# Performance work log

Measured on AMD Instinct MI355X. Metric: run time of the kernel, lower is better.

## Reference

```python
import jax, jax.numpy as jnp
import numpy as np

DIM = 768
HEADS = 12
HEAD_DIM = DIM // HEADS
EPS = 1e-5

def setup_inputs() -> dict:
    key = jax.random.key(0)
    ks = jax.random.split(key, 12)
    s = 1.0 / np.sqrt(DIM)
    x = jax.random.normal(ks[0], (4, 2048, DIM), dtype=jnp.float32)
    Wq = jax.random.uniform(ks[1], (DIM, DIM), jnp.float32, -s, s)
    bq = jnp.zeros((DIM,), jnp.float32)
    Wk = jax.random.uniform(ks[2], (DIM, DIM), jnp.float32, -s, s)
    bk = jnp.zeros((DIM,), jnp.float32)
    Wv = jax.random.uniform(ks[3], (DIM, DIM), jnp.float32, -s, s)
    bv = jnp.zeros((DIM,), jnp.float32)
    W1 = jax.random.uniform(ks[4], (DIM, 2 * DIM), jnp.float32, -s, s)
    b1 = jnp.zeros((2 * DIM,), jnp.float32)
    s2 = 1.0 / np.sqrt(2 * DIM)
    W2 = jax.random.uniform(ks[5], (2 * DIM, DIM), jnp.float32, -s2, s2)
    b2 = jnp.zeros((DIM,), jnp.float32)
    gamma = jnp.ones((DIM,), jnp.float32)
    beta = jnp.zeros((DIM,), jnp.float32)
    return {"x": x, "Wq": Wq, "bq": bq, "Wk": Wk, "bk": bk, "Wv": Wv, "bv": bv,
            "W1": W1, "b1": b1, "W2": W2, "b2": b2, "gamma": gamma, "beta": beta}

def reference(x, Wq, bq, Wk, bk, Wv, bv, W1, b1, W2, b2, gamma, beta):
    B, S, _ = x.shape
    # QKV projections -> (B, H, S, Dh)
    q = (x @ Wq + bq).reshape(B, S, HEADS, HEAD_DIM).transpose(0, 2, 1, 3)
    k = (x @ Wk + bk).reshape(B, S, HEADS, HEAD_DIM).transpose(0, 2, 1, 3)
    v = (x @ Wv + bv).reshape(B, S, HEADS, HEAD_DIM).transpose(0, 2, 1, 3)
    scores = jnp.einsum('bhqd,bhkd->bhqk', q, k) / jnp.sqrt(jnp.float32(HEAD_DIM))
    attn = jax.nn.softmax(scores, axis=-1)  # dropout is identity in eval
    ctx = jnp.einsum('bhqk,bhkd->bhqd', attn, v)
    ctx = ctx.transpose(0, 2, 1, 3).reshape(B, S, DIM)
    # MLP
    out = jax.nn.relu(ctx @ W1 + b1) @ W2 + b2
    # residual + LayerNorm
    h = x + out
    mu = jnp.mean(h, axis=-1, keepdims=True)
    var = jnp.mean(jnp.square(h - mu), axis=-1, keepdims=True)
    return (h - mu) * jax.lax.rsqrt(var + EPS) * gamma + beta
```

## Files before the change

### kernel.cpp

```cpp
#include <hip/hip_runtime.h>
#include <stdint.h>

#define DIM 768
#define HDIM 64
#define NHEADS 12
#define SEQ 2048
#define BATCH 4
#define NTOK (BATCH*SEQ)
#define FF 1536
#define QSCALE 0.1803368801111204f

typedef __bf16 bf16x8 __attribute__((ext_vector_type(8)));
typedef float f32x4 __attribute__((ext_vector_type(4)));
typedef unsigned short u16;
typedef unsigned int u32;

static __device__ __forceinline__ u16 f2bf(float f) {
  u32 u = __float_as_uint(f);
  u32 r = (u + 0x7fffu + ((u >> 16) & 1u)) >> 16;
  return (u16)r;
}

static __device__ __forceinline__ void async16(const void* g, void* l) {
  __builtin_amdgcn_global_load_lds(
      (const __attribute__((address_space(1))) u32*)g,
      (__attribute__((address_space(3))) u32*)l, 16, 0, 0);
}


__global__ void conv_bf16(const float* __restrict__ in, u16* __restrict__ out, int n) {
  int i = (blockIdx.x * 256 + threadIdx.x) * 4;
  if (i < n) {
    float4 f = *(const float4*)(in + i);
    uint2 o;
    o.x = (u32)f2bf(f.x) | ((u32)f2bf(f.y) << 16);
    o.y = (u32)f2bf(f.z) | ((u32)f2bf(f.w) << 16);
    *(uint2*)(out + i) = o;
  }
}

__global__ void transp_bf16(const float* __restrict__ W, u16* __restrict__ Wt, int K, int N) {
  __shared__ float tile[32][33];
  const int k0 = blockIdx.x * 32, n0 = blockIdx.y * 32;
  const int tx = threadIdx.x & 31, ty = threadIdx.x >> 5;
#pragma unroll
  for (int i = 0; i < 4; i++)
    tile[ty + 8 * i][tx] = W[(size_t)(k0 + ty + 8 * i) * N + n0 + tx];
  __syncthreads();
#pragma unroll
  for (int i = 0; i < 4; i++)
    Wt[(size_t)(n0 + ty + 8 * i) * K + k0 + tx] = f2bf(tile[tx][ty + 8 * i]);
}

__global__ void transp_qkv(const float* __restrict__ Wq, const float* __restrict__ Wk,
                           const float* __restrict__ Wv, u16* __restrict__ Wt) {
  __shared__ float tile[32][33];
  const float* W = blockIdx.z == 0 ? Wq : (blockIdx.z == 1 ? Wk : Wv);
  u16* dst = Wt + (size_t)blockIdx.z * DIM * DIM;
  const int k0 = blockIdx.x * 32, n0 = blockIdx.y * 32;
  const int tx = threadIdx.x & 31, ty = threadIdx.x >> 5;
#pragma unroll
  for (int i = 0; i < 4; i++)
    tile[ty + 8 * i][tx] = W[(size_t)(k0 + ty + 8 * i) * DIM + n0 + tx];
  __syncthreads();
#pragma unroll
  for (int i = 0; i < 4; i++)
    dst[(size_t)(n0 + ty + 8 * i) * DIM + k0 + tx] = f2bf(tile[tx][ty + 8 * i]);
}

__global__ void concat_bias(const float* __restrict__ a, const float* __restrict__ b,
                            const float* __restrict__ c, float* __restrict__ o) {
  int i = blockIdx.x * 256 + threadIdx.x;
  if (i < DIM) o[i] = a[i];
  else if (i < 2 * DIM) o[i] = b[i - DIM];
  else if (i < 3 * DIM) o[i] = c[i - 2 * DIM];
}


template<int MODE>
__launch_bounds__(256, 3)
__global__ void gemm128(const u16* __restrict__ A, const u16* __restrict__ Bt,
                        const float* __restrict__ bias, void* __restrict__ outp,
                        int K) {
  __shared__ u16 sA[128 * 64];
  __shared__ u16 sB[128 * 64];
  const int t = threadIdx.x;
  const int w = t >> 6;
  const int lane = t & 63;
  const int quad = lane >> 4;
  const int l15 = lane & 15;
  const int m0 = blockIdx.x * 128;
  const int n0 = blockIdx.y * 128;
  const int wr = (w & 1) * 64;
  const int wc = (w >> 1) * 64;

  f32x4 acc[4][4];
#pragma unroll
  for (int i = 0; i < 4; i++)
#pragma unroll
    for (int j = 0; j < 4; j++) acc[i][j] = (f32x4){0.f, 0.f, 0.f, 0.f};

  const int rowA = lane >> 3;
  const int colSw = ((lane & 7) ^ rowA) * 8;

  for (int k0 = 0; k0 < K; k0 += 64) {
    __syncthreads();
#pragma unroll
    for (int j = 0; j < 4; j++) {
      int r0 = (j * 4 + w) * 8;
      async16(A + (size_t)(m0 + r0 + rowA) * K + k0 + colSw, sA + r0 * 64);
      async16(Bt + (size_t)(n0 + r0 + rowA) * K + k0 + colSw, sB + r0 * 64);
    }
    __builtin_amdgcn_s_waitcnt(0);
    __syncthreads();
#pragma unroll
    for (int ks = 0; ks < 64; ks += 32) {
      bf16x8 a[4], b[4];
#pragma unroll
      for (int i = 0; i < 4; i++)
        a[i] = *(const bf16x8*)(sA + (wr + i * 16 + l15) * 64 +
                                ((((ks >> 3) + quad) ^ (l15 & 7)) * 8));
#pragma unroll
      for (int j = 0; j < 4; j++)
        b[j] = *(const bf16x8*)(sB + (wc + j * 16 + l15) * 64 +
                                ((((ks >> 3) + quad) ^ (l15 & 7)) * 8));
#pragma unroll
      for (int i = 0; i < 4; i++)
#pragma unroll
        for (int j = 0; j < 4; j++)
          acc[i][j] = __builtin_amdgcn_mfma_f32_16x16x32_bf16(a[i], b[j], acc[i][j], 0, 0, 0);
    }
  }

#pragma unroll
  for (int i = 0; i < 4; i++) {
#pragma unroll
    for (int j = 0; j < 4; j++) {
#pragma unroll
      for (int r = 0; r < 4; r++) {
        int m = m0 + wr + i * 16 + quad * 4 + r;
        int n = n0 + wc + j * 16 + l15;
        float v = acc[i][j][r] + bias[n];
        if (MODE == 5) {
          int b = m >> 11, s = m & 2047;
          u16* o = (u16*)outp;
          if (n < DIM) {
            int h = n >> 6, d = n & 63;
            o[(((size_t)(b * NHEADS + h) * SEQ + s) << 6) + d] = f2bf(v * QSCALE);
          } else if (n < 2 * DIM) {
            int nn = n - DIM, h = nn >> 6, d = nn & 63;
            o[(size_t)NTOK * DIM + (((size_t)(b * NHEADS + h) * SEQ + s) << 6) + d] = f2bf(v);
          } else {
            int nn = n - 2 * DIM, h = nn >> 6, d = nn & 63;
            o[2 * (size_t)NTOK * DIM + ((size_t)(b * NHEADS + h) * HDIM + d) * SEQ + s] = f2bf(v);
          }
        } else if (MODE == 3) {
          ((u16*)outp)[(size_t)m * FF + n] = f2bf(fmaxf(v, 0.f));
        } else {
          ((float*)outp)[(size_t)m * DIM + n] = v;
        }
      }
    }
  }
}


__launch_bounds__(256, 4)
__global__ void attn(const u16* __restrict__ Q, const u16* __restrict__ Kb,
                     const u16* __restrict__ Vt, u16* __restrict__ Ctx) {
  __shared__ u16 sK[128 * 64];
  __shared__ u16 sV[64 * 128];
  __shared__ u16 sP[4][16 * 64];
  const int t = threadIdx.x, w = t >> 6, lane = t & 63;
  const int quad = lane >> 4, l15 = lane & 15;
  const int qtile = blockIdx.x;
  const int bh = blockIdx.y;
  const size_t qkbase = (size_t)bh * SEQ * HDIM;
  const int q0 = qtile * 64 + w * 16;

  bf16x8 qf[2];
#pragma unroll
  for (int ks = 0; ks < 2; ks++)
    qf[ks] = *(const bf16x8*)(Q + qkbase + (size_t)(q0 + l15) * HDIM + ks * 32 + quad * 8);

  f32x4 o[4];
#pragma unroll
  for (int i = 0; i < 4; i++) o[i] = (f32x4){0.f, 0.f, 0.f, 0.f};
  float rs[4] = {0.f, 0.f, 0.f, 0.f};

  const int rowK = lane >> 3;
  const int colKsw = ((lane & 7) ^ rowK) * 8;
  const int rowVl = lane >> 4;
  const int chV = lane & 15;
  const int hi = l15 >> 3;

  for (int kt = 0; kt < SEQ / 128; kt++) {
    __syncthreads();
#pragma unroll
    for (int j = 0; j < 4; j++) {
      int rk = (j * 4 + w) * 8;
      async16(Kb + qkbase + (size_t)(kt * 128 + rk + rowK) * HDIM + colKsw, sK + rk * 64);
      int rv = (j * 4 + w) * 4;
      int rV = rv + rowVl;
      int cV = (chV ^ (rV & 15)) * 8;
      async16(Vt + qkbase + (size_t)rV * SEQ + kt * 128 + cV, sV + rv * 128);
    }
    __builtin_amdgcn_s_waitcnt(0);
    __syncthreads();

    u16* pw = sP[w];
#pragma unroll
    for (int hh = 0; hh < 2; hh++) {
      f32x4 sc[4];
#pragma unroll
      for (int n4 = 0; n4 < 4; n4++) {
        int ni = hh * 4 + n4;
        f32x4 c = (f32x4){0.f, 0.f, 0.f, 0.f};
        bf16x8 b0 = *(const bf16x8*)(sK + (ni * 16 + l15) * 64 + ((quad ^ (l15 & 7)) * 8));
        bf16x8 b1 = *(const bf16x8*)(sK + (ni * 16 + l15) * 64 + (((4 + quad) ^ (l15 & 7)) * 8));
        c = __builtin_amdgcn_mfma_f32_16x16x32_bf16(qf[0], b0, c, 0, 0, 0);
        c = __builtin_amdgcn_mfma_f32_16x16x32_bf16(qf[1], b1, c, 0, 0, 0);
        sc[n4] = c;
      }
#pragma unroll
      for (int r = 0; r < 4; r++) {
        int prow = quad * 4 + r;
        u16* prb = pw + prow * 64 + (l15 & 7);
#pragma unroll
        for (int n4 = 0; n4 < 4; n4++) {
          float p = __builtin_amdgcn_exp2f(sc[n4][r]);
          rs[r] += p;
          prb[(((n4 * 2 + hi) ^ (prow & 7)) * 8)] = (u16)((__float_as_uint(p) + 0x8000u) >> 16);
        }
      }
#pragma unroll
      for (int ks = 0; ks < 2; ks++) {
        bf16x8 a = *(const bf16x8*)(pw + l15 * 64 + (((ks * 4 + quad) ^ (l15 & 7)) * 8));
#pragma unroll
        for (int di = 0; di < 4; di++) {
          bf16x8 b = *(const bf16x8*)(sV + (di * 16 + l15) * 128 +
                                      (((hh * 8 + ks * 4 + quad) ^ l15) * 8));
          o[di] = __builtin_amdgcn_mfma_f32_16x16x32_bf16(a, b, o[di], 0, 0, 0);
        }
      }
    }
  }

  int b = bh / NHEADS, h = bh - b * NHEADS;
#pragma unroll
  for (int r = 0; r < 4; r++) {
    float s = rs[r];
#pragma unroll
    for (int off = 1; off < 16; off <<= 1) s += __shfl_xor(s, off);
    float inv = 1.f / s;
    int sq = q0 + quad * 4 + r;
    size_t base = (size_t)(b * SEQ + sq) * DIM + h * HDIM;
#pragma unroll
    for (int di = 0; di < 4; di++)
      Ctx[base + di * 16 + l15] = f2bf(o[di][r] * inv);
  }
}


__launch_bounds__(64)
__global__ void ln_kernel(const float* __restrict__ x, const float* __restrict__ y,
                          const float* __restrict__ gamma, const float* __restrict__ beta,
                          float* __restrict__ out) {
  const int tok = blockIdx.x;
  const int lane = threadIdx.x;
  const float4* X = (const float4*)(x + (size_t)tok * DIM);
  const float4* Y = (const float4*)(y + (size_t)tok * DIM);
  const float4* G = (const float4*)gamma;
  const float4* Bt = (const float4*)beta;
  float4* O = (float4*)(out + (size_t)tok * DIM);

  float4 h[3];
  float s = 0.f;
#pragma unroll
  for (int i = 0; i < 3; i++) {
    float4 a = X[i * 64 + lane], b = Y[i * 64 + lane];
    h[i].x = a.x + b.x; h[i].y = a.y + b.y; h[i].z = a.z + b.z; h[i].w = a.w + b.w;
    s += h[i].x + h[i].y + h[i].z + h[i].w;
  }
#pragma unroll
  for (int off = 32; off >= 1; off >>= 1) s += __shfl_xor(s, off);
  float mu = s * (1.f / DIM);
  float v = 0.f;
#pragma unroll
  for (int i = 0; i < 3; i++) {
    h[i].x -= mu; h[i].y -= mu; h[i].z -= mu; h[i].w -= mu;
    v += h[i].x * h[i].x + h[i].y * h[i].y + h[i].z * h[i].z + h[i].w * h[i].w;
  }
#pragma unroll
  for (int off = 32; off >= 1; off >>= 1) v += __shfl_xor(v, off);
  float rstd = rsqrtf(v * (1.f / DIM) + 1e-5f);
#pragma unroll
  for (int i = 0; i < 3; i++) {
    float4 g = G[i * 64 + lane], bt = Bt[i * 64 + lane];
    float4 r;
    r.x = h[i].x * rstd * g.x + bt.x;
    r.y = h[i].y * rstd * g.y + bt.y;
    r.z = h[i].z * rstd * g.z + bt.z;
    r.w = h[i].w * rstd * g.w + bt.w;
    O[i * 64 + lane] = r;
  }
}


extern "C" void kernel_launch(void* const* d_in, const int* in_sizes, int n_in,
                              void* d_out, int out_size, void* d_ws, size_t ws_size,
                              hipStream_t stream) {
  const float* x  = (const float*)d_in[0];
  const float* Wq = (const float*)d_in[1];
  const float* bq = (const float*)d_in[2];
  const float* Wk = (const float*)d_in[3];
  const float* bk = (const float*)d_in[4];
  const float* Wv = (const float*)d_in[5];
  const float* bv = (const float*)d_in[6];
  const float* W1 = (const float*)d_in[7];
  const float* b1 = (const float*)d_in[8];
  const float* W2 = (const float*)d_in[9];
  const float* b2 = (const float*)d_in[10];
  const float* gamma = (const float*)d_in[11];
  const float* beta  = (const float*)d_in[12];

  char* ws = (char*)d_ws;
  u16* xb   = (u16*)ws;           ws += (size_t)NTOK * DIM * 2;
  u16* Wqkvt = (u16*)ws;          ws += (size_t)DIM * DIM * 3 * 2;
  u16* W1t  = (u16*)ws;           ws += (size_t)DIM * FF * 2;
  u16* W2t  = (u16*)ws;           ws += (size_t)DIM * FF * 2;
  float* bqkv = (float*)ws;       ws += (size_t)3 * DIM * 4;
  u16* Qb   = (u16*)ws;           ws += (size_t)NTOK * DIM * 2;
  u16* Kbf  = (u16*)ws;           ws += (size_t)NTOK * DIM * 2;
  u16* Vtb  = (u16*)ws;           ws += (size_t)NTOK * DIM * 2;
  u16* Ctx  = (u16*)ws;           ws += (size_t)NTOK * DIM * 2;
  u16* H1   = (u16*)ws;           ws += (size_t)NTOK * FF * 2;
  float* Y2 = (float*)ws;         ws += (size_t)NTOK * DIM * 4;

  conv_bf16<<<(NTOK * DIM) / 1024, 256, 0, stream>>>(x, xb, NTOK * DIM);
  transp_qkv<<<dim3(DIM / 32, DIM / 32, 3), 256, 0, stream>>>(Wq, Wk, Wv, Wqkvt);
  transp_bf16<<<dim3(DIM / 32, FF / 32), 256, 0, stream>>>(W1, W1t, DIM, FF);
  transp_bf16<<<dim3(FF / 32, DIM / 32), 256, 0, stream>>>(W2, W2t, FF, DIM);
  concat_bias<<<9, 256, 0, stream>>>(bq, bk, bv, bqkv);

  gemm128<5><<<dim3(NTOK / 128, 3 * DIM / 128), 256, 0, stream>>>(xb, Wqkvt, bqkv, Qb, DIM);

  attn<<<dim3(SEQ / 64, BATCH * NHEADS), 256, 0, stream>>>(Qb, Kbf, Vtb, Ctx);

  gemm128<3><<<dim3(NTOK / 128, FF / 128), 256, 0, stream>>>(Ctx, W1t, b1, H1, DIM);
  gemm128<4><<<dim3(NTOK / 128, DIM / 128), 256, 0, stream>>>(H1, W2t, b2, Y2, FF);

  ln_kernel<<<NTOK, 64, 0, stream>>>(x, Y2, gamma, beta, (float*)d_out);
}
```

Measured before the change: 308.9 us.

## Double attention query tile per wave and remap blocks to XCDs by head

Each wave now handles 32 query rows instead of 16, so each K/V tile loaded into LDS is reused across twice as many queries. The QK^T product is transposed (K as A operand) so P can be written to LDS with packed 64-bit stores, and row sums are reduced with fewer shuffles. The grid is flattened, and each head's query blocks are mapped to the same XCD so they can share K/V in L2. The cost is more registers and LDS, reflected in lowering launch bounds occupancy from 4 to 3, and half as many blocks.

```diff
diff --git a/kernel.cpp b/kernel.cpp
--- a/kernel.cpp
+++ b/kernel.cpp
@@ -165,34 +165,43 @@
 }
 
 
-__launch_bounds__(256, 4)
+__launch_bounds__(256, 3)
 __global__ void attn(const u16* __restrict__ Q, const u16* __restrict__ Kb,
                      const u16* __restrict__ Vt, u16* __restrict__ Ctx) {
   __shared__ u16 sK[128 * 64];
   __shared__ u16 sV[64 * 128];
-  __shared__ u16 sP[4][16 * 64];
+  __shared__ u16 sP[4][32 * 64];
   const int t = threadIdx.x, w = t >> 6, lane = t & 63;
   const int quad = lane >> 4, l15 = lane & 15;
-  const int qtile = blockIdx.x;
-  const int bh = blockIdx.y;
+
+  const int fid = blockIdx.x;
+  const int xcd = fid & 7;
+  const int idx = fid >> 3;
+  const int bh = xcd + 8 * (idx >> 4);
+  const int qb = idx & 15;
   const size_t qkbase = (size_t)bh * SEQ * HDIM;
-  const int q0 = qtile * 64 + w * 16;
-
-  bf16x8 qf[2];
-#pragma unroll
-  for (int ks = 0; ks < 2; ks++)
-    qf[ks] = *(const bf16x8*)(Q + qkbase + (size_t)(q0 + l15) * HDIM + ks * 32 + quad * 8);
-
-  f32x4 o[4];
-#pragma unroll
-  for (int i = 0; i < 4; i++) o[i] = (f32x4){0.f, 0.f, 0.f, 0.f};
-  float rs[4] = {0.f, 0.f, 0.f, 0.f};
+  const int q0 = qb * 128 + w * 32;
+
+  bf16x8 qf[2][2];
+#pragma unroll
+  for (int i = 0; i < 2; i++)
+#pragma unroll
+    for (int ks = 0; ks < 2; ks++)
+      qf[i][ks] = *(const bf16x8*)(Q + qkbase + (size_t)(q0 + i * 16 + l15) * HDIM +
+                                   ks * 32 + quad * 8);
+
+  f32x4 o[2][4];
+#pragma unroll
+  for (int i = 0; i < 2; i++)
+#pragma unroll
+    for (int di = 0; di < 4; di++) o[i][di] = (f32x4){0.f, 0.f, 0.f, 0.f};
+  float rs[2] = {0.f, 0.f};
 
   const int rowK = lane >> 3;
   const int colKsw = ((lane & 7) ^ rowK) * 8;
   const int rowVl = lane >> 4;
   const int chV = lane & 15;
-  const int hi = l15 >> 3;
+  const int swz = l15 & 7;
 
   for (int kt = 0; kt < SEQ / 128; kt++) {
     __syncthreads();
@@ -211,53 +220,78 @@
     u16* pw = sP[w];
 #pragma unroll
     for (int hh = 0; hh < 2; hh++) {
-      f32x4 sc[4];
+      f32x4 sc[2][4];
 #pragma unroll
       for (int n4 = 0; n4 < 4; n4++) {
-        int ni = hh * 4 + n4;
-        f32x4 c = (f32x4){0.f, 0.f, 0.f, 0.f};
-        bf16x8 b0 = *(const bf16x8*)(sK + (ni * 16 + l15) * 64 + ((quad ^ (l15 & 7)) * 8));
-        bf16x8 b1 = *(const bf16x8*)(sK + (ni * 16 + l15) * 64 + (((4 + quad) ^ (l15 & 7)) * 8));
-        c = __builtin_amdgcn_mfma_f32_16x16x32_bf16(qf[0], b0, c, 0, 0, 0);
-        c = __builtin_amdgcn_mfma_f32_16x16x32_bf16(qf[1], b1, c, 0, 0, 0);
-        sc[n4] = c;
+        int kr = (hh * 4 + n4) * 16;
+        bf16x8 a0 = *(const bf16x8*)(sK + (kr + l15) * 64 + ((quad ^ swz) * 8));
+        bf16x8 a1 = *(const bf16x8*)(sK + (kr + l15) * 64 + (((4 + quad) ^ swz) * 8));
+#pragma unroll
+        for (int i = 0; i < 2; i++) {
+          f32x4 c = (f32x4){0.f, 0.f, 0.f, 0.f};
+          c = __builtin_amdgcn_mfma_f32_16x16x32_bf16(a0, qf[i][0], c, 0, 0, 0);
+          c = __builtin_amdgcn_mfma_f32_16x16x32_bf16(a1, qf[i][1], c, 0, 0, 0);
+          sc[i][n4] = c;
+        }
       }
 #pragma unroll
-      for (int r = 0; r < 4; r++) {
-        int prow = quad * 4 + r;
-        u16* prb = pw + prow * 64 + (l15 & 7);
+      for (int i = 0; i < 2; i++) {
+        int row = i * 16 + l15;
 #pragma unroll
         for (int n4 = 0; n4 < 4; n4++) {
-          float p = __builtin_amdgcn_exp2f(sc[n4][r]);
-          rs[r] += p;
-          prb[(((n4 * 2 + hi) ^ (prow & 7)) * 8)] = (u16)((__float_as_uint(p) + 0x8000u) >> 16);
+          float p0 = __builtin_amdgcn_exp2f(sc[i][n4][0]);
+          float p1 = __builtin_amdgcn_exp2f(sc[i][n4][1]);
+          float p2 = __builtin_amdgcn_exp2f(sc[i][n4][2]);
+          float p3 = __builtin_amdgcn_exp2f(sc[i][n4][3]);
+          rs[i] += (p0 + p1) + (p2 + p3);
+          u32 lo = ((__float_as_uint(p0) + 0x8000u) >> 16) |
+                   ((__float_as_uint(p1) + 0x8000u) & 0xffff0000u);
+          u32 hi = ((__float_as_uint(p2) + 0x8000u) >> 16) |
+                   ((__float_as_uint(p3) + 0x8000u) & 0xffff0000u);
+          int cp = (n4 * 2 + (quad >> 1)) ^ swz;
+          *(uint2*)(pw + row * 64 + cp * 8 + (quad & 1) * 4) = (uint2){lo, hi};
         }
       }
 #pragma unroll
       for (int ks = 0; ks < 2; ks++) {
-        bf16x8 a = *(const bf16x8*)(pw + l15 * 64 + (((ks * 4 + quad) ^ (l15 & 7)) * 8));
+        bf16x8 ap[2];
+#pragma unroll
+        for (int i = 0; i < 2; i++) {
+          int row = i * 16 + l15;
+          int cp = (ks * 4 + quad) ^ swz;
+          ap[i] = *(const bf16x8*)(pw + row * 64 + cp * 8);
+        }
 #pragma unroll
         for (int di = 0; di < 4; di++) {
           bf16x8 b = *(const bf16x8*)(sV + (di * 16 + l15) * 128 +
                                       (((hh * 8 + ks * 4 + quad) ^ l15) * 8));
-          o[di] = __builtin_amdgcn_mfma_f32_16x16x32_bf16(a, b, o[di], 0, 0, 0);
+          o[0][di] = __builtin_amdgcn_mfma_f32_16x16x32_bf16(ap[0], b, o[0][di], 0, 0, 0);
+          o[1][di] = __builtin_amdgcn_mfma_f32_16x16x32_bf16(ap[1], b, o[1][di], 0, 0, 0);
         }
       }
     }
   }
 
+  float rsum[2];
+#pragma unroll
+  for (int i = 0; i < 2; i++) {
+    float s = rs[i];
+    s += __shfl_xor(s, 16);
+    s += __shfl_xor(s, 32);
+    rsum[i] = s;
+  }
   int b = bh / NHEADS, h = bh - b * NHEADS;
 #pragma unroll
-  for (int r = 0; r < 4; r++) {
-    float s = rs[r];
-#pragma unroll
-    for (int off = 1; off < 16; off <<= 1) s += __shfl_xor(s, off);
-    float inv = 1.f / s;
-    int sq = q0 + quad * 4 + r;
-    size_t base = (size_t)(b * SEQ + sq) * DIM + h * HDIM;
-#pragma unroll
-    for (int di = 0; di < 4; di++)
-      Ctx[base + di * 16 + l15] = f2bf(o[di][r] * inv);
+  for (int i = 0; i < 2; i++) {
+#pragma unroll
+    for (int r = 0; r < 4; r++) {
+      float inv = 1.f / __shfl(rsum[i], quad * 4 + r);
+      int q = q0 + i * 16 + quad * 4 + r;
+      size_t base = (size_t)(b * SEQ + q) * DIM + h * HDIM;
+#pragma unroll
+      for (int di = 0; di < 4; di++)
+        Ctx[base + di * 16 + l15] = f2bf(o[i][di][r] * inv);
+    }
   }
 }
 
@@ -345,7 +379,7 @@
 
   gemm128<5><<<dim3(NTOK / 128, 3 * DIM / 128), 256, 0, stream>>>(xb, Wqkvt, bqkv, Qb, DIM);
 
-  attn<<<dim3(SEQ / 64, BATCH * NHEADS), 256, 0, stream>>>(Qb, Kbf, Vtb, Ctx);
+  attn<<<768, 256, 0, stream>>>(Qb, Kbf, Vtb, Ctx);
 
   gemm128<3><<<dim3(NTOK / 128, FF / 128), 256, 0, stream>>>(Ctx, W1t, b1, H1, DIM);
   gemm128<4><<<dim3(NTOK / 128, DIM / 128), 256, 0, stream>>>(H1, W2t, b2, Y2, FF);
```

Measured after the change: 311.2 us. No clear change (+0.7%).
